# Kernel tuning notes

Hardware: AMD Instinct MI355X
Metric: run time of the kernel (lower is better)

## Reference

```python
import jax, jax.numpy as jnp
import numpy as np

EPS = 1e-6
N_NFT, N_TRADER, D = 16384, 8192, 8
NNZ = 2_000_000


def setup_inputs() -> dict:
    key = jax.random.key(0)
    k1, k2, k3, k4, k5, k6, k7 = jax.random.split(key, 7)
    return {
        "latent_z": jax.random.normal(k1, (N_NFT, D), dtype=jnp.float32),
        "latent_q": jax.random.normal(k2, (N_TRADER, D), dtype=jnp.float32),
        "gamma": jax.random.normal(k3, (N_NFT,), dtype=jnp.float32),
        "delta": jax.random.normal(k4, (N_TRADER,), dtype=jnp.float32),
        "weights": jax.random.uniform(k5, (NNZ,), dtype=jnp.float32),
        "sparse_i": jax.random.randint(k6, (NNZ,), 0, N_NFT, dtype=jnp.int64) if jax.config.jax_enable_x64 else jax.random.randint(k6, (NNZ,), 0, N_NFT, dtype=jnp.int32),
        "sparse_j": jax.random.randint(k7, (NNZ,), 0, N_TRADER, dtype=jnp.int32),
    }


def reference(latent_z, latent_q, gamma, delta, weights, sparse_i, sparse_j):
    # --- dense normalizer: exp(gamma)^T @ exp(-(cdist(z+eps, q)+eps)) @ exp(delta)
    z = latent_z + EPS  # torch.cdist(self.latent_z + 1e-6, self.latent_q)
    zn = jnp.sum(z * z, axis=-1)                     # [N]
    qn = jnp.sum(latent_q * latent_q, axis=-1)       # [M]
    d2 = zn[:, None] + qn[None, :] - 2.0 * (z @ latent_q.T)  # [N, M]
    dist = jnp.sqrt(jnp.maximum(d2, 0.0))
    mat = jnp.exp(-(dist + EPS))                     # [N, M]
    z_pdist1 = jnp.exp(gamma) @ mat @ jnp.exp(delta)  # scalar

    # --- sparse Poisson log-likelihood term over observed edges
    diff = latent_z[sparse_i] - latent_q[sparse_j] + EPS  # [nnz, D]
    zqdist = -jnp.sqrt(jnp.sum(diff * diff, axis=-1))     # [nnz]
    z_pdist2 = jnp.sum(weights * (gamma[sparse_i] + delta[sparse_j] + zqdist))

    return z_pdist2 - z_pdist1
```

## Files before the change

### kernel.cpp

```cpp
#include <hip/hip_runtime.h>

#define EPSF 1e-6f
#define L2E  1.44269504088896340736f

using bf16x8 = __attribute__((ext_vector_type(8))) short;
using f32x16 = __attribute__((ext_vector_type(16))) float;

constexpr int NT   = 256;
constexpr int JC   = 256;
constexpr int NJC  = 8192 / JC;
constexpr int RPAN = 128;
constexpr int NRP  = 16384 / RPAN;
constexpr int NB   = NRP * NJC;
constexpr int JT   = JC / 32;

__device__ __forceinline__ short f2bf(float f) {
    union { float f; unsigned u; } c{f};
    return (short)((c.u + 0x7fffu + ((c.u >> 16) & 1u)) >> 16);
}
__device__ __forceinline__ float bf2f(short s) {
    union { unsigned u; float f; } c{((unsigned)(unsigned short)s) << 16};
    return c.f;
}

__device__ __forceinline__ float block_reduce_sum(float v) {
#pragma unroll
    for (int off = 32; off > 0; off >>= 1) v += __shfl_down(v, off, 64);
    __shared__ float parts[4];
    const int t = threadIdx.x;
    if ((t & 63) == 0) parts[t >> 6] = v;
    __syncthreads();
    float r = 0.f;
    if (t == 0) r = parts[0] + parts[1] + parts[2] + parts[3];
    return r;
}

__global__ __launch_bounds__(NT) void fused_kernel(
    const float* __restrict__ z, const float* __restrict__ q,
    const float* __restrict__ gamma, const float* __restrict__ delta,
    const float* __restrict__ w, const int* __restrict__ si,
    const int* __restrict__ sj, int nnz, float* __restrict__ partial)
{
    __shared__ short sza[RPAN * 16];
    __shared__ float seg[RPAN];
    __shared__ short sqb[JC * 16];
    __shared__ float sed[JC];

    const int t    = threadIdx.x;
    const int id   = blockIdx.x;
    const int jc   = id & (NJC - 1);
    const int rpan = id >> 5;
    const int c0   = jc * JC;

    if (t < RPAN) {
        const int row = rpan * RPAN + t;
        const float4 a = *(const float4*)(z + (size_t)row * 8);
        const float4 b = *(const float4*)(z + (size_t)row * 8 + 4);
        const float h[8] = {L2E * (a.x + EPSF), L2E * (a.y + EPSF),
                            L2E * (a.z + EPSF), L2E * (a.w + EPSF),
                            L2E * (b.x + EPSF), L2E * (b.y + EPSF),
                            L2E * (b.z + EPSF), L2E * (b.w + EPSF)};
        float zn = 0.f;
#pragma unroll
        for (int d = 0; d < 8; ++d) {
            const short s = f2bf(h[d]);
            sza[t * 16 + d] = s;
            const float r = bf2f(s);
            zn = fmaf(r, r, zn);
        }
        sza[t * 16 + 8] = f2bf(zn);
        sza[t * 16 + 9] = (short)0x3F80;
#pragma unroll
        for (int d = 10; d < 16; ++d) sza[t * 16 + d] = 0;
        seg[t] = __expf(gamma[row]);
    }

    {
        const int C = c0 + t;
        const float4 a = *(const float4*)(q + (size_t)C * 8);
        const float4 b = *(const float4*)(q + (size_t)C * 8 + 4);
        const float h[8] = {L2E * a.x, L2E * a.y, L2E * a.z, L2E * a.w,
                            L2E * b.x, L2E * b.y, L2E * b.z, L2E * b.w};
        float qn = 0.f;
#pragma unroll
        for (int d = 0; d < 8; ++d) {
            const short s = f2bf(h[d]);
            const float r = bf2f(s);
            qn = fmaf(r, r, qn);
            sqb[t * 16 + d] = f2bf(-2.f * r);
        }
        sqb[t * 16 + 8] = (short)0x3F80;
        sqb[t * 16 + 9] = f2bf(qn);
#pragma unroll
        for (int d = 10; d < 16; ++d) sqb[t * 16 + d] = 0;
        sed[t] = __expf(delta[C] - EPSF);
    }

    float sacc = 0.f;
    for (int k = id * NT + t; k < nnz; k += NB * NT) {
        const int i = si[k];
        const int j = sj[k];
        const float4 a = *(const float4*)(z + (size_t)i * 8);
        const float4 b = *(const float4*)(z + (size_t)i * 8 + 4);
        const float4 c = *(const float4*)(q + (size_t)j * 8);
        const float4 d = *(const float4*)(q + (size_t)j * 8 + 4);
        const float d0 = a.x - c.x + EPSF, d1 = a.y - c.y + EPSF;
        const float d2 = a.z - c.z + EPSF, d3 = a.w - c.w + EPSF;
        const float d4 = b.x - d.x + EPSF, d5 = b.y - d.y + EPSF;
        const float d6 = b.z - d.z + EPSF, d7 = b.w - d.w + EPSF;
        float s2 = d0 * d0;
        s2 = fmaf(d1, d1, s2); s2 = fmaf(d2, d2, s2); s2 = fmaf(d3, d3, s2);
        s2 = fmaf(d4, d4, s2); s2 = fmaf(d5, d5, s2); s2 = fmaf(d6, d6, s2);
        s2 = fmaf(d7, d7, s2);
        const float dist = __builtin_amdgcn_sqrtf(s2);
        sacc = fmaf(w[k], gamma[i] + delta[j] - dist, sacc);
    }
    __syncthreads();

    const int wv   = t >> 6;
    const int lane = t & 63;
    const int li   = lane & 31;
    const int half = lane >> 5;

    const bf16x8 afrag = *(const bf16x8*)&sza[(wv * 32 + li) * 16 + half * 8];
    const short* bp    = &sqb[li * 16 + half * 8];
    const float* edp   = &sed[li];

    float acc[16];
#pragma unroll
    for (int r = 0; r < 16; ++r) acc[r] = 0.f;

#pragma unroll
    for (int jt = 0; jt < JT; ++jt) {
        const bf16x8 bfrag = *(const bf16x8*)(bp + jt * 32 * 16);
        const float  ed_l  = edp[jt * 32];
        f32x16 s = __builtin_amdgcn_mfma_f32_32x32x16_bf16(
            afrag, bfrag, (f32x16)(0.f), 0, 0, 0);
#pragma unroll
        for (int r = 0; r < 16; ++r) {
            const float d2 = fmaxf(s[r], 0.f);
            const float st = __builtin_amdgcn_sqrtf(d2);
            acc[r] = fmaf(ed_l, __builtin_amdgcn_exp2f(-st), acc[r]);
        }
    }

    float vv = 0.f;
#pragma unroll
    for (int r4 = 0; r4 < 4; ++r4)
#pragma unroll
        for (int r0 = 0; r0 < 4; ++r0)
            vv = fmaf(seg[wv * 32 + half * 4 + r0 + 8 * r4], acc[r4 * 4 + r0], vv);

    const float v = block_reduce_sum(sacc - vv);
    if (t == 0) partial[id] = v;
}

__global__ __launch_bounds__(256) void reduce_kernel(
    const float* __restrict__ partial, int n, float* __restrict__ out)
{
    float v = 0.f;
    for (int k = threadIdx.x; k < n; k += 256) v += partial[k];
    v = block_reduce_sum(v);
    if (threadIdx.x == 0) out[0] = v;
}

extern "C" void kernel_launch(void* const* d_in, const int* in_sizes, int n_in,
                              void* d_out, int out_size, void* d_ws, size_t ws_size,
                              hipStream_t stream) {
    const float* z     = (const float*)d_in[0];
    const float* q     = (const float*)d_in[1];
    const float* gamma = (const float*)d_in[2];
    const float* delta = (const float*)d_in[3];
    const float* w     = (const float*)d_in[4];
    const int*   si    = (const int*)d_in[5];
    const int*   sj    = (const int*)d_in[6];
    const int    nnz   = in_sizes[4];

    float* out = (float*)d_out;
    float* ws  = (float*)d_ws;

    fused_kernel<<<NB, NT, 0, stream>>>(z, q, gamma, delta, w, si, sj, nnz, ws);
    reduce_kernel<<<1, 256, 0, stream>>>(ws, NB, out);
}
```

Measured before the change: 51.76 us.

## Widen column chunk, build A fragments in registers, fold delta into exp2

Doubles the per-block column chunk to 512, so there are half as many blocks and each does twice the MFMA tiles. The z-side A fragment is now built directly in registers from global memory instead of being staged through shared memory. exp(delta) is folded into the exp2 argument as a log2-scaled add, which turns an FMA into an add. fmaxf is replaced by fabs before the sqrt, which assumes negative squared distances are tiny rounding errors. In exchange, fewer blocks mean less parallelism for the sparse gather loop, and the fabs substitution slightly changes numerics for near-zero distances.

```diff
diff --git a/kernel.cpp b/kernel.cpp
--- a/kernel.cpp
+++ b/kernel.cpp
@@ -7,12 +7,13 @@
 using f32x16 = __attribute__((ext_vector_type(16))) float;
 
 constexpr int NT   = 256;
-constexpr int JC   = 256;
+constexpr int JC   = 512;
 constexpr int NJC  = 8192 / JC;
 constexpr int RPAN = 128;
 constexpr int NRP  = 16384 / RPAN;
 constexpr int NB   = NRP * NJC;
 constexpr int JT   = JC / 32;
+constexpr int RSTR = 16;
 
 __device__ __forceinline__ short f2bf(float f) {
     union { float f; unsigned u; } c{f};
@@ -35,48 +36,54 @@
     return r;
 }
 
+__device__ __forceinline__ bf16x8 make_afrag(const float* __restrict__ z,
+                                             int row, int half) {
+    const float4 a = *(const float4*)(z + (size_t)row * 8);
+    const float4 b = *(const float4*)(z + (size_t)row * 8 + 4);
+    const float h[8] = {L2E * (a.x + EPSF), L2E * (a.y + EPSF),
+                        L2E * (a.z + EPSF), L2E * (a.w + EPSF),
+                        L2E * (b.x + EPSF), L2E * (b.y + EPSF),
+                        L2E * (b.z + EPSF), L2E * (b.w + EPSF)};
+    short s[8];
+    float zn = 0.f;
+#pragma unroll
+    for (int d = 0; d < 8; ++d) {
+        s[d] = f2bf(h[d]);
+        const float r = bf2f(s[d]);
+        zn = fmaf(r, r, zn);
+    }
+    bf16x8 f;
+    if (half == 0) {
+        f[0] = s[0]; f[1] = s[1]; f[2] = s[2]; f[3] = s[3];
+        f[4] = s[4]; f[5] = s[5]; f[6] = s[6]; f[7] = s[7];
+    } else {
+        f[0] = f2bf(zn); f[1] = (short)0x3F80;
+        f[2] = 0; f[3] = 0; f[4] = 0; f[5] = 0; f[6] = 0; f[7] = 0;
+    }
+    return f;
+}
+
 __global__ __launch_bounds__(NT) void fused_kernel(
     const float* __restrict__ z, const float* __restrict__ q,
     const float* __restrict__ gamma, const float* __restrict__ delta,
     const float* __restrict__ w, const int* __restrict__ si,
     const int* __restrict__ sj, int nnz, float* __restrict__ partial)
 {
-    __shared__ short sza[RPAN * 16];
+    __shared__ short sqb[JC * RSTR];
+    __shared__ float sld[JC];
     __shared__ float seg[RPAN];
-    __shared__ short sqb[JC * 16];
-    __shared__ float sed[JC];
 
-    const int t    = threadIdx.x;
-    const int id   = blockIdx.x;
-    const int jc   = id & (NJC - 1);
-    const int rpan = id >> 5;
-    const int c0   = jc * JC;
+    const int t      = threadIdx.x;
+    const int id     = blockIdx.x;
+    const int jc     = id & (NJC - 1);
+    const int rpan   = id >> 4;
+    const int c0     = jc * JC;
+    const int r0base = rpan * RPAN;
 
-    if (t < RPAN) {
-        const int row = rpan * RPAN + t;
-        const float4 a = *(const float4*)(z + (size_t)row * 8);
-        const float4 b = *(const float4*)(z + (size_t)row * 8 + 4);
-        const float h[8] = {L2E * (a.x + EPSF), L2E * (a.y + EPSF),
-                            L2E * (a.z + EPSF), L2E * (a.w + EPSF),
-                            L2E * (b.x + EPSF), L2E * (b.y + EPSF),
-                            L2E * (b.z + EPSF), L2E * (b.w + EPSF)};
-        float zn = 0.f;
+    if (t < RPAN) seg[t] = __expf(gamma[r0base + t]);
 #pragma unroll
-        for (int d = 0; d < 8; ++d) {
-            const short s = f2bf(h[d]);
-            sza[t * 16 + d] = s;
-            const float r = bf2f(s);
-            zn = fmaf(r, r, zn);
-        }
-        sza[t * 16 + 8] = f2bf(zn);
-        sza[t * 16 + 9] = (short)0x3F80;
-#pragma unroll
-        for (int d = 10; d < 16; ++d) sza[t * 16 + d] = 0;
-        seg[t] = __expf(gamma[row]);
-    }
-
-    {
-        const int C = c0 + t;
+    for (int c = t; c < JC; c += NT) {
+        const int C = c0 + c;
         const float4 a = *(const float4*)(q + (size_t)C * 8);
         const float4 b = *(const float4*)(q + (size_t)C * 8 + 4);
         const float h[8] = {L2E * a.x, L2E * a.y, L2E * a.z, L2E * a.w,
@@ -87,14 +94,20 @@
             const short s = f2bf(h[d]);
             const float r = bf2f(s);
             qn = fmaf(r, r, qn);
-            sqb[t * 16 + d] = f2bf(-2.f * r);
+            sqb[c * RSTR + d] = f2bf(-2.f * r);
         }
-        sqb[t * 16 + 8] = (short)0x3F80;
-        sqb[t * 16 + 9] = f2bf(qn);
+        sqb[c * RSTR + 8] = (short)0x3F80;
+        sqb[c * RSTR + 9] = f2bf(qn);
 #pragma unroll
-        for (int d = 10; d < 16; ++d) sqb[t * 16 + d] = 0;
-        sed[t] = __expf(delta[C] - EPSF);
+        for (int d = 10; d < 16; ++d) sqb[c * RSTR + d] = 0;
+        sld[c] = L2E * (delta[C] - EPSF);
     }
+
+    const int wv   = t >> 6;
+    const int lane = t & 63;
+    const int li   = lane & 31;
+    const int half = lane >> 5;
+    const bf16x8 afrag = make_afrag(z, r0base + wv * 32 + li, half);
 
     float sacc = 0.f;
     for (int k = id * NT + t; k < nnz; k += NB * NT) {
@@ -112,19 +125,9 @@
         s2 = fmaf(d1, d1, s2); s2 = fmaf(d2, d2, s2); s2 = fmaf(d3, d3, s2);
         s2 = fmaf(d4, d4, s2); s2 = fmaf(d5, d5, s2); s2 = fmaf(d6, d6, s2);
         s2 = fmaf(d7, d7, s2);
-        const float dist = __builtin_amdgcn_sqrtf(s2);
-        sacc = fmaf(w[k], gamma[i] + delta[j] - dist, sacc);
+        sacc = fmaf(w[k], gamma[i] + delta[j] - __builtin_amdgcn_sqrtf(s2), sacc);
     }
     __syncthreads();
-
-    const int wv   = t >> 6;
-    const int lane = t & 63;
-    const int li   = lane & 31;
-    const int half = lane >> 5;
-
-    const bf16x8 afrag = *(const bf16x8*)&sza[(wv * 32 + li) * 16 + half * 8];
-    const short* bp    = &sqb[li * 16 + half * 8];
-    const float* edp   = &sed[li];
 
     float acc[16];
 #pragma unroll
@@ -132,15 +135,14 @@
 
 #pragma unroll
     for (int jt = 0; jt < JT; ++jt) {
-        const bf16x8 bfrag = *(const bf16x8*)(bp + jt * 32 * 16);
-        const float  ed_l  = edp[jt * 32];
+        const bf16x8 bfrag = *(const bf16x8*)&sqb[(jt * 32 + li) * RSTR + half * 8];
+        const float  ld_l  = sld[jt * 32 + li];
         f32x16 s = __builtin_amdgcn_mfma_f32_32x32x16_bf16(
             afrag, bfrag, (f32x16)(0.f), 0, 0, 0);
 #pragma unroll
         for (int r = 0; r < 16; ++r) {
-            const float d2 = fmaxf(s[r], 0.f);
-            const float st = __builtin_amdgcn_sqrtf(d2);
-            acc[r] = fmaf(ed_l, __builtin_amdgcn_exp2f(-st), acc[r]);
+            const float st = __builtin_amdgcn_sqrtf(__builtin_fabsf(s[r]));
+            acc[r] += __builtin_amdgcn_exp2f(ld_l - st);
         }
     }
 
```

After: 48.03 us. -7.2%, faster.
